# Kernel optimization log

Hardware: AMD Instinct MI355X
Metric: run time of the kernel (lower is better)

## Reference

```python
import jax, jax.numpy as jnp
import numpy as np

MARGIN = 0.3
N, D = 8192, 256
NUM_IDS = 1000


def setup_inputs() -> dict:
    key = jax.random.key(0)
    k1, k2 = jax.random.split(key)
    inputs = jax.random.normal(k1, (N, D), dtype=jnp.float32)
    targets = jax.random.randint(k2, (N,), 0, NUM_IDS, dtype=jnp.int64)
    return {"inputs": inputs, "targets": targets}


def reference(inputs, targets):
    # sim_mat[i, j] = <x_i, x_j>
    sim = jnp.matmul(inputs, inputs.T)  # [n, n]
    same = targets[:, None] == targets[None, :]  # [n, n] bool
    # positives: same label AND sim < 1 (note: strict; diagonal included only if ||x||^2 < 1)
    pos_mask = same & (sim < 1.0)
    # negatives: different label AND sim > margin
    neg_mask = (~same) & (sim > MARGIN)
    pos_loss = jnp.sum(jnp.where(pos_mask, 1.0 - sim, 0.0), axis=1)  # [n]
    neg_loss = jnp.sum(jnp.where(neg_mask, sim, 0.0), axis=1)  # [n]
    n = inputs.shape[0]
    return jnp.sum(pos_loss + neg_loss) / n
```

## Files before the change

### kernel.cpp

```cpp
#include <hip/hip_runtime.h>
#include <hip/hip_bf16.h>


#define NROWS 8192
#define DDIM  256
#define MARGINF 0.3f

typedef __attribute__((ext_vector_type(8))) short short8x;
typedef __attribute__((ext_vector_type(4))) float f32x4;

__device__ __forceinline__ unsigned short f2bf(float f) {
    unsigned int u = __float_as_uint(f);
    unsigned int r = (u + 0x7fffu + ((u >> 16) & 1u)) >> 16;
    return (unsigned short)r;
}

__global__ void __launch_bounds__(256) convert_k(const float* __restrict__ x,
                                                 unsigned short* __restrict__ xb) {
    int i = blockIdx.x * 256 + threadIdx.x;
    const float4* p = reinterpret_cast<const float4*>(x) + (size_t)i * 2;
    float4 a = p[0];
    float4 b = p[1];
    short8x o;
    o[0] = (short)f2bf(a.x); o[1] = (short)f2bf(a.y);
    o[2] = (short)f2bf(a.z); o[3] = (short)f2bf(a.w);
    o[4] = (short)f2bf(b.x); o[5] = (short)f2bf(b.y);
    o[6] = (short)f2bf(b.z); o[7] = (short)f2bf(b.w);
    reinterpret_cast<short8x*>(xb)[i] = o;
}

__global__ void __launch_bounds__(256) gemm_loss_k(const unsigned short* __restrict__ xb,
                                                   const int* __restrict__ tg,
                                                   double* __restrict__ partials) {
    const int p = blockIdx.x;
    int bi = (int)(64.5f - sqrtf(64.5f * 64.5f - 2.0f * (float)p));
    if (bi < 0) bi = 0;
    if (bi > 63) bi = 63;
    while (bi > 0 && (bi * (129 - bi)) / 2 > p) --bi;
    while (((bi + 1) * (128 - bi)) / 2 <= p) ++bi;
    const int bj = bi + (p - (bi * (129 - bi)) / 2);

    __shared__ unsigned short lA[2][128 * 64];
    __shared__ unsigned short lB[2][128 * 64];
    __shared__ int lti[128];
    __shared__ int ltj[128];
    __shared__ float redbuf[4];

    const int tid  = threadIdx.x;
    const int lane = tid & 63;
    const int wid  = tid >> 6;
    const int wr   = wid >> 1;
    const int wc   = wid & 1;

    if (tid < 128)       lti[tid]        = tg[bi * 128 + tid];
    else                 ltj[tid - 128]  = tg[bj * 128 + (tid - 128)];

    const int lrow   = lane >> 3;
    const int schunk = ((lane & 7) ^ lrow) << 4;

    const char* aBase = (const char*)(xb + (size_t)bi * 128 * 256);
    const char* bBase = (const char*)(xb + (size_t)bj * 128 * 256);

    const int g   = lane >> 4;
    const int x7  = lane & 7;
    const int rA  = wr * 64 + (lane & 15);
    const int rB  = wc * 64 + (lane & 15);
    int aoff[2], arow[4], brow[4];
#pragma unroll
    for (int kk = 0; kk < 2; ++kk) aoff[kk] = (((kk * 4 + g) ^ x7) << 3);
#pragma unroll
    for (int m = 0; m < 4; ++m) { arow[m] = (rA + m * 16) * 64; brow[m] = (rB + m * 16) * 64; }

    f32x4 acc[4][4] = {};

    auto STAGE = [&](int buf, int ks) {
        const int k0b = ks * 128;
#pragma unroll
        for (int t = 0; t < 4; ++t) {
            const int issue = wid * 4 + t;
            const int r = issue * 8 + lrow;
            const char* sa = aBase + (size_t)r * 512 + k0b + schunk;
            const char* sb = bBase + (size_t)r * 512 + k0b + schunk;
            __builtin_amdgcn_global_load_lds(
                (const __attribute__((address_space(1))) unsigned int*)sa,
                (__attribute__((address_space(3))) unsigned int*)&lA[buf][issue * 512],
                16, 0, 0);
            __builtin_amdgcn_global_load_lds(
                (const __attribute__((address_space(1))) unsigned int*)sb,
                (__attribute__((address_space(3))) unsigned int*)&lB[buf][issue * 512],
                16, 0, 0);
        }
    };

    STAGE(0, 0);
    __syncthreads();

    int buf = 0;
#pragma unroll
    for (int ks = 0; ks < 4; ++ks) {
        if (ks < 3) STAGE(buf ^ 1, ks + 1);

        const unsigned short* la = lA[buf];
        const unsigned short* lb = lB[buf];
#pragma unroll
        for (int kk = 0; kk < 2; ++kk) {
            short8x af[4], bf[4];
#pragma unroll
            for (int m = 0; m < 4; ++m)
                af[m] = *(const short8x*)&la[arow[m] + aoff[kk]];
#pragma unroll
            for (int n = 0; n < 4; ++n)
                bf[n] = *(const short8x*)&lb[brow[n] + aoff[kk]];
#pragma unroll
            for (int m = 0; m < 4; ++m)
#pragma unroll
                for (int n = 0; n < 4; ++n)
                    acc[m][n] = __builtin_amdgcn_mfma_f32_16x16x32_bf16(
                        af[m], bf[n], acc[m][n], 0, 0, 0);
        }

        if (ks < 3) { __syncthreads(); buf ^= 1; }
    }

    const int colbase = wc * 64 + (lane & 15);
    int tjv[4];
#pragma unroll
    for (int n = 0; n < 4; ++n) tjv[n] = ltj[colbase + n * 16];

    float lsum = 0.f;
    if (bi != bj) {
#pragma unroll
        for (int m = 0; m < 4; ++m) {
#pragma unroll
            for (int r = 0; r < 4; ++r) {
                const int ti = lti[wr * 64 + m * 16 + (g << 2) + r];
#pragma unroll
                for (int n = 0; n < 4; ++n) {
                    const float s = acc[m][n][r];
                    const float posv = fmaxf(1.0f - s, 0.0f);
                    const float negv = (s > MARGINF) ? s : 0.0f;
                    lsum += (ti == tjv[n]) ? posv : negv;
                }
            }
        }
        lsum *= 2.0f;
    } else {
#pragma unroll
        for (int m = 0; m < 4; ++m) {
#pragma unroll
            for (int r = 0; r < 4; ++r) {
                const int rl = wr * 64 + m * 16 + (g << 2) + r;
                const int ti = lti[rl];
#pragma unroll
                for (int n = 0; n < 4; ++n) {
                    const int cl = colbase + n * 16;
                    const float s = acc[m][n][r];
                    const float posv = fmaxf(1.0f - s, 0.0f);
                    const float negv = (s > MARGINF) ? s : 0.0f;
                    const float c = (ti == tjv[n]) ? posv : negv;
                    const float w = (cl > rl) ? 2.0f : ((cl == rl) ? 1.0f : 0.0f);
                    lsum += w * c;
                }
            }
        }
    }

#pragma unroll
    for (int mask = 1; mask < 64; mask <<= 1) lsum += __shfl_xor(lsum, mask, 64);
    if (lane == 0) redbuf[wid] = lsum;
    __syncthreads();
    if (tid == 0)
        partials[p] = (double)(redbuf[0] + redbuf[1] + redbuf[2] + redbuf[3]);
}

__global__ void __launch_bounds__(256) finalize_k(const double* __restrict__ partials,
                                                  float* __restrict__ out) {
    double s = 0.0;
    for (int i = threadIdx.x; i < 2080; i += 256) s += partials[i];
#pragma unroll
    for (int mask = 1; mask < 64; mask <<= 1) s += __shfl_xor(s, mask, 64);
    __shared__ double red[4];
    const int wid = threadIdx.x >> 6;
    if ((threadIdx.x & 63) == 0) red[wid] = s;
    __syncthreads();
    if (threadIdx.x == 0)
        out[0] = (float)((red[0] + red[1] + red[2] + red[3]) / 8192.0);
}

extern "C" void kernel_launch(void* const* d_in, const int* in_sizes, int n_in,
                              void* d_out, int out_size, void* d_ws, size_t ws_size,
                              hipStream_t stream) {
    (void)in_sizes; (void)n_in; (void)out_size; (void)ws_size;
    const float* x  = (const float*)d_in[0];
    const int*   tg = (const int*)d_in[1];
    float* out = (float*)d_out;

    double* partials   = (double*)d_ws;
    unsigned short* xb = (unsigned short*)((char*)d_ws + 32768);

    convert_k<<<1024, 256, 0, stream>>>(x, xb);
    gemm_loss_k<<<2080, 256, 0, stream>>>(xb, tg, partials);
    finalize_k<<<1, 256, 0, stream>>>(partials, out);
}
```

Baseline: 95.15 us.

## Enlarge GEMM tile to 256x256 with 8 waves and MFMA priority hints

Each block now computes a 256x256 upper-triangular tile with 512 threads, each wave holding an 8x4 grid of MFMA accumulators. The grid shrinks from 2080 blocks to 528, and the partial-sum reduction is resized to match. The goal is to cut global and LDS traffic per FLOP through more operand reuse. The change also raises wave priority around the MFMA loop and puts the rare same-label case on a predicted-unlikely branch in the loss epilogue. In exchange, each block needs 128KB of LDS, which likely allows only one block per CU, and 528 blocks may spread unevenly across the CUs.

```diff
diff --git a/kernel.cpp b/kernel.cpp
--- a/kernel.cpp
+++ b/kernel.cpp
@@ -29,49 +29,49 @@
     reinterpret_cast<short8x*>(xb)[i] = o;
 }
 
-__global__ void __launch_bounds__(256) gemm_loss_k(const unsigned short* __restrict__ xb,
-                                                   const int* __restrict__ tg,
-                                                   double* __restrict__ partials) {
+__global__ void __launch_bounds__(512, 2) gemm_loss_k(const unsigned short* __restrict__ xb,
+                                                      const int* __restrict__ tg,
+                                                      double* __restrict__ partials) {
     const int p = blockIdx.x;
-    int bi = (int)(64.5f - sqrtf(64.5f * 64.5f - 2.0f * (float)p));
+    int bi = (int)(32.5f - sqrtf(32.5f * 32.5f - 2.0f * (float)p));
     if (bi < 0) bi = 0;
-    if (bi > 63) bi = 63;
-    while (bi > 0 && (bi * (129 - bi)) / 2 > p) --bi;
-    while (((bi + 1) * (128 - bi)) / 2 <= p) ++bi;
-    const int bj = bi + (p - (bi * (129 - bi)) / 2);
-
-    __shared__ unsigned short lA[2][128 * 64];
-    __shared__ unsigned short lB[2][128 * 64];
-    __shared__ int lti[128];
-    __shared__ int ltj[128];
-    __shared__ float redbuf[4];
+    if (bi > 31) bi = 31;
+    while (bi > 0 && (bi * (65 - bi)) / 2 > p) --bi;
+    while (((bi + 1) * (64 - bi)) / 2 <= p) ++bi;
+    const int bj = bi + (p - (bi * (65 - bi)) / 2);
+
+    __shared__ unsigned short lA[2][256 * 64];
+    __shared__ unsigned short lB[2][256 * 64];
+    __shared__ int lti[256];
+    __shared__ int ltj[256];
+    __shared__ float redbuf[8];
 
     const int tid  = threadIdx.x;
     const int lane = tid & 63;
     const int wid  = tid >> 6;
-    const int wr   = wid >> 1;
-    const int wc   = wid & 1;
-
-    if (tid < 128)       lti[tid]        = tg[bi * 128 + tid];
-    else                 ltj[tid - 128]  = tg[bj * 128 + (tid - 128)];
+    const int wr   = wid >> 2;
+    const int wc   = wid & 3;
+
+    if (tid < 256)       lti[tid]        = tg[bi * 256 + tid];
+    else                 ltj[tid - 256]  = tg[bj * 256 + (tid - 256)];
 
     const int lrow   = lane >> 3;
     const int schunk = ((lane & 7) ^ lrow) << 4;
 
-    const char* aBase = (const char*)(xb + (size_t)bi * 128 * 256);
-    const char* bBase = (const char*)(xb + (size_t)bj * 128 * 256);
-
-    const int g   = lane >> 4;
-    const int x7  = lane & 7;
-    const int rA  = wr * 64 + (lane & 15);
-    const int rB  = wc * 64 + (lane & 15);
-    int aoff[2], arow[4], brow[4];
-#pragma unroll
-    for (int kk = 0; kk < 2; ++kk) aoff[kk] = (((kk * 4 + g) ^ x7) << 3);
-#pragma unroll
-    for (int m = 0; m < 4; ++m) { arow[m] = (rA + m * 16) * 64; brow[m] = (rB + m * 16) * 64; }
-
-    f32x4 acc[4][4] = {};
+    const char* aBase = (const char*)(xb + (size_t)bi * 256 * 256);
+    const char* bBase = (const char*)(xb + (size_t)bj * 256 * 256);
+
+    const int g  = lane >> 4;
+    const int x7 = lane & 7;
+    int koff[2], arow[8], brow[4];
+#pragma unroll
+    for (int kk = 0; kk < 2; ++kk) koff[kk] = (((kk * 4 + g) ^ x7) << 3);
+#pragma unroll
+    for (int m = 0; m < 8; ++m) arow[m] = (wr * 128 + m * 16 + (lane & 15)) * 64;
+#pragma unroll
+    for (int n = 0; n < 4; ++n) brow[n] = (wc * 64 + n * 16 + (lane & 15)) * 64;
+
+    f32x4 acc[8][4] = {};
 
     auto STAGE = [&](int buf, int ks) {
         const int k0b = ks * 128;
@@ -104,19 +104,21 @@
         const unsigned short* lb = lB[buf];
 #pragma unroll
         for (int kk = 0; kk < 2; ++kk) {
-            short8x af[4], bf[4];
-#pragma unroll
-            for (int m = 0; m < 4; ++m)
-                af[m] = *(const short8x*)&la[arow[m] + aoff[kk]];
+            short8x af[8], bf[4];
+#pragma unroll
+            for (int m = 0; m < 8; ++m)
+                af[m] = *(const short8x*)&la[arow[m] + koff[kk]];
 #pragma unroll
             for (int n = 0; n < 4; ++n)
-                bf[n] = *(const short8x*)&lb[brow[n] + aoff[kk]];
-#pragma unroll
-            for (int m = 0; m < 4; ++m)
+                bf[n] = *(const short8x*)&lb[brow[n] + koff[kk]];
+            __builtin_amdgcn_s_setprio(1);
+#pragma unroll
+            for (int m = 0; m < 8; ++m)
 #pragma unroll
                 for (int n = 0; n < 4; ++n)
                     acc[m][n] = __builtin_amdgcn_mfma_f32_16x16x32_bf16(
                         af[m], bf[n], acc[m][n], 0, 0, 0);
+            __builtin_amdgcn_s_setprio(0);
         }
 
         if (ks < 3) { __syncthreads(); buf ^= 1; }
@@ -130,26 +132,27 @@
     float lsum = 0.f;
     if (bi != bj) {
 #pragma unroll
-        for (int m = 0; m < 4; ++m) {
+        for (int m = 0; m < 8; ++m) {
 #pragma unroll
             for (int r = 0; r < 4; ++r) {
-                const int ti = lti[wr * 64 + m * 16 + (g << 2) + r];
+                const int ti = lti[wr * 128 + m * 16 + (g << 2) + r];
 #pragma unroll
                 for (int n = 0; n < 4; ++n) {
                     const float s = acc[m][n][r];
-                    const float posv = fmaxf(1.0f - s, 0.0f);
                     const float negv = (s > MARGINF) ? s : 0.0f;
-                    lsum += (ti == tjv[n]) ? posv : negv;
+                    lsum += negv;
+                    if (__builtin_expect(ti == tjv[n], 0))
+                        lsum += fmaxf(1.0f - s, 0.0f) - negv;
                 }
             }
         }
         lsum *= 2.0f;
     } else {
 #pragma unroll
-        for (int m = 0; m < 4; ++m) {
+        for (int m = 0; m < 8; ++m) {
 #pragma unroll
             for (int r = 0; r < 4; ++r) {
-                const int rl = wr * 64 + m * 16 + (g << 2) + r;
+                const int rl = wr * 128 + m * 16 + (g << 2) + r;
                 const int ti = lti[rl];
 #pragma unroll
                 for (int n = 0; n < 4; ++n) {
@@ -169,14 +172,18 @@
     for (int mask = 1; mask < 64; mask <<= 1) lsum += __shfl_xor(lsum, mask, 64);
     if (lane == 0) redbuf[wid] = lsum;
     __syncthreads();
-    if (tid == 0)
-        partials[p] = (double)(redbuf[0] + redbuf[1] + redbuf[2] + redbuf[3]);
+    if (tid == 0) {
+        float t = 0.f;
+#pragma unroll
+        for (int w = 0; w < 8; ++w) t += redbuf[w];
+        partials[p] = (double)t;
+    }
 }
 
 __global__ void __launch_bounds__(256) finalize_k(const double* __restrict__ partials,
                                                   float* __restrict__ out) {
     double s = 0.0;
-    for (int i = threadIdx.x; i < 2080; i += 256) s += partials[i];
+    for (int i = threadIdx.x; i < 528; i += 256) s += partials[i];
 #pragma unroll
     for (int mask = 1; mask < 64; mask <<= 1) s += __shfl_xor(s, mask, 64);
     __shared__ double red[4];
@@ -199,6 +206,6 @@
     unsigned short* xb = (unsigned short*)((char*)d_ws + 32768);
 
     convert_k<<<1024, 256, 0, stream>>>(x, xb);
-    gemm_loss_k<<<2080, 256, 0, stream>>>(xb, tg, partials);
+    gemm_loss_k<<<528, 512, 0, stream>>>(xb, tg, partials);
     finalize_k<<<1, 256, 0, stream>>>(partials, out);
 }
```

Measured after the change: 98.99 us. 4.0% more time.

## Pre-swizzle bf16 operands into MFMA fragment order and load directly from global

Applied to the files above, without the earlier changes.

The convert kernel now writes the bf16 copy of the input in a layout that matches the per-lane MFMA fragment order, in 16-row by 32-column groups. The GEMM kernel drops its LDS double buffering and global_load_lds staging and reads each fragment straight from global memory as one contiguous 16-byte load per lane. Launch bounds now request 3 blocks per CU. This removes LDS traffic and the barriers between k-steps, but operand reuse now depends on L1/L2 caching and there is no explicit prefetch overlapping loads with MFMA work.

```diff
diff --git a/kernel.cpp b/kernel.cpp
--- a/kernel.cpp
+++ b/kernel.cpp
@@ -2,8 +2,6 @@
 #include <hip/hip_bf16.h>
 
 
-#define NROWS 8192
-#define DDIM  256
 #define MARGINF 0.3f
 
 typedef __attribute__((ext_vector_type(8))) short short8x;
@@ -17,21 +15,26 @@
 
 __global__ void __launch_bounds__(256) convert_k(const float* __restrict__ x,
                                                  unsigned short* __restrict__ xb) {
-    int i = blockIdx.x * 256 + threadIdx.x;
-    const float4* p = reinterpret_cast<const float4*>(x) + (size_t)i * 2;
-    float4 a = p[0];
-    float4 b = p[1];
+    int u = blockIdx.x * 256 + threadIdx.x;
+    int lane = u & 63;
+    int kk   = (u >> 6) & 7;
+    int r16  = u >> 9;
+    int row  = r16 * 16 + (lane & 15);
+    int col  = kk * 32 + (lane >> 4) * 8;
+    const float4* src = reinterpret_cast<const float4*>(x + (size_t)row * 256 + col);
+    float4 a = src[0];
+    float4 b = src[1];
     short8x o;
     o[0] = (short)f2bf(a.x); o[1] = (short)f2bf(a.y);
     o[2] = (short)f2bf(a.z); o[3] = (short)f2bf(a.w);
     o[4] = (short)f2bf(b.x); o[5] = (short)f2bf(b.y);
     o[6] = (short)f2bf(b.z); o[7] = (short)f2bf(b.w);
-    reinterpret_cast<short8x*>(xb)[i] = o;
+    reinterpret_cast<short8x*>(xb)[u] = o;
 }
 
-__global__ void __launch_bounds__(256) gemm_loss_k(const unsigned short* __restrict__ xb,
-                                                   const int* __restrict__ tg,
-                                                   double* __restrict__ partials) {
+__global__ void __launch_bounds__(256, 3) gemm_loss_k(const unsigned short* __restrict__ xb,
+                                                      const int* __restrict__ tg,
+                                                      double* __restrict__ partials) {
     const int p = blockIdx.x;
     int bi = (int)(64.5f - sqrtf(64.5f * 64.5f - 2.0f * (float)p));
     if (bi < 0) bi = 0;
@@ -40,8 +43,6 @@
     while (((bi + 1) * (128 - bi)) / 2 <= p) ++bi;
     const int bj = bi + (p - (bi * (129 - bi)) / 2);
 
-    __shared__ unsigned short lA[2][128 * 64];
-    __shared__ unsigned short lB[2][128 * 64];
     __shared__ int lti[128];
     __shared__ int ltj[128];
     __shared__ float redbuf[4];
@@ -54,74 +55,30 @@
 
     if (tid < 128)       lti[tid]        = tg[bi * 128 + tid];
     else                 ltj[tid - 128]  = tg[bj * 128 + (tid - 128)];
+    __syncthreads();
 
-    const int lrow   = lane >> 3;
-    const int schunk = ((lane & 7) ^ lrow) << 4;
-
-    const char* aBase = (const char*)(xb + (size_t)bi * 128 * 256);
-    const char* bBase = (const char*)(xb + (size_t)bj * 128 * 256);
-
-    const int g   = lane >> 4;
-    const int x7  = lane & 7;
-    const int rA  = wr * 64 + (lane & 15);
-    const int rB  = wc * 64 + (lane & 15);
-    int aoff[2], arow[4], brow[4];
-#pragma unroll
-    for (int kk = 0; kk < 2; ++kk) aoff[kk] = (((kk * 4 + g) ^ x7) << 3);
-#pragma unroll
-    for (int m = 0; m < 4; ++m) { arow[m] = (rA + m * 16) * 64; brow[m] = (rB + m * 16) * 64; }
+    const short8x* xf = reinterpret_cast<const short8x*>(xb);
+    const int aIdx = (bi * 8 + wr * 4) * 512 + lane;
+    const int bIdx = (bj * 8 + wc * 4) * 512 + lane;
 
     f32x4 acc[4][4] = {};
 
-    auto STAGE = [&](int buf, int ks) {
-        const int k0b = ks * 128;
 #pragma unroll
-        for (int t = 0; t < 4; ++t) {
-            const int issue = wid * 4 + t;
-            const int r = issue * 8 + lrow;
-            const char* sa = aBase + (size_t)r * 512 + k0b + schunk;
-            const char* sb = bBase + (size_t)r * 512 + k0b + schunk;
-            __builtin_amdgcn_global_load_lds(
-                (const __attribute__((address_space(1))) unsigned int*)sa,
-                (__attribute__((address_space(3))) unsigned int*)&lA[buf][issue * 512],
-                16, 0, 0);
-            __builtin_amdgcn_global_load_lds(
-                (const __attribute__((address_space(1))) unsigned int*)sb,
-                (__attribute__((address_space(3))) unsigned int*)&lB[buf][issue * 512],
-                16, 0, 0);
-        }
-    };
-
-    STAGE(0, 0);
-    __syncthreads();
-
-    int buf = 0;
+    for (int kk = 0; kk < 8; ++kk) {
+        short8x af[4], bf[4];
 #pragma unroll
-    for (int ks = 0; ks < 4; ++ks) {
-        if (ks < 3) STAGE(buf ^ 1, ks + 1);
-
-        const unsigned short* la = lA[buf];
-        const unsigned short* lb = lB[buf];
+        for (int n = 0; n < 4; ++n) bf[n] = xf[bIdx + n * 512 + kk * 64];
 #pragma unroll
-        for (int kk = 0; kk < 2; ++kk) {
-            short8x af[4], bf[4];
+        for (int m = 0; m < 4; ++m) af[m] = xf[aIdx + m * 512 + kk * 64];
 #pragma unroll
-            for (int m = 0; m < 4; ++m)
-                af[m] = *(const short8x*)&la[arow[m] + aoff[kk]];
+        for (int m = 0; m < 4; ++m)
 #pragma unroll
             for (int n = 0; n < 4; ++n)
-                bf[n] = *(const short8x*)&lb[brow[n] + aoff[kk]];
-#pragma unroll
-            for (int m = 0; m < 4; ++m)
-#pragma unroll
-                for (int n = 0; n < 4; ++n)
-                    acc[m][n] = __builtin_amdgcn_mfma_f32_16x16x32_bf16(
-                        af[m], bf[n], acc[m][n], 0, 0, 0);
-        }
-
-        if (ks < 3) { __syncthreads(); buf ^= 1; }
+                acc[m][n] = __builtin_amdgcn_mfma_f32_16x16x32_bf16(
+                    af[m], bf[n], acc[m][n], 0, 0, 0);
     }
 
+    const int g = lane >> 4;
     const int colbase = wc * 64 + (lane & 15);
     int tjv[4];
 #pragma unroll
```

Result: faster. 92.25 us (-3.1%).
